# Performance work log

Measured on AMD Instinct MI355X. Metric: run time of the kernel, lower is better.

The kernel has to match this reference:

```python
import math
import jax, jax.numpy as jnp
import numpy as np

B = 32768
DM = 256      # d_model
DS = 16       # d_state
DI = 256      # d_inner (expand=1)
DTR = 16      # dt_rank = ceil(256/16)
FF = 512      # FFN hidden


def setup_inputs() -> dict:
    key = jax.random.key(0)
    ks = jax.random.split(key, 10)
    def rn(k, sh, s=0.02):
        return jax.random.normal(k, sh, jnp.float32) * s
    return {
        "x_0": jax.random.uniform(ks[0], (B, 4), jnp.float32),
        "flow_features": jax.random.normal(ks[1], (B, 1, DM), jnp.float32),
        "h": jnp.zeros((B, DI, DS), jnp.float32),
        "W_in": rn(ks[2], (2 * DI, DM)),
        "W_x": rn(ks[3], (DTR + 2 * DS, DI)),
        "W_dt": rn(ks[4], (DI, DTR)),
        "b_dt": jnp.zeros((DI,), jnp.float32),
        "A_log": jnp.log(jnp.broadcast_to(jnp.arange(1, DS + 1, dtype=jnp.float32), (DI, DS))),
        "D": jnp.ones((DI,), jnp.float32),
        "W1": rn(ks[5], (FF, DM)),
        "b1": jnp.zeros((FF,), jnp.float32),
        "W2": rn(ks[6], (DM, FF)),
        "b2": jnp.zeros((DM,), jnp.float32),
        "gamma": jnp.ones((DM,), jnp.float32),
        "beta": jnp.zeros((DM,), jnp.float32),
        "W_bb": rn(ks[7], (4, DM)),
        "b_bb": jnp.zeros((4,), jnp.float32),
    }


def _sine_embed(pos, dim_per_axis):
    # Matches gen_sineembed_for_position for pos.shape[-1]==4 (cx, cy, w, h order)
    dim_t = 10000.0 ** (2.0 * (jnp.arange(dim_per_axis) // 2).astype(jnp.float32) / dim_per_axis)
    scale = 2.0 * math.pi
    def emb(v):  # v: (b,)
        p = v[:, None] * scale / dim_t          # (b, dim)
        return jnp.stack([jnp.sin(p[:, 0::2]), jnp.cos(p[:, 1::2])], axis=2).reshape(v.shape[0], dim_per_axis)
    return jnp.concatenate([emb(pos[:, 0]), emb(pos[:, 1]), emb(pos[:, 2]), emb(pos[:, 3])], axis=1)


def reference(x_0, flow_features, h, W_in, W_x, W_dt, b_dt, A_log, D,
              W1, b1, W2, b2, gamma, beta, W_bb, b_bb):
    # 1) sinusoidal bbox embedding -> (b, d_model)
    pos = _sine_embed(x_0, DM // 4)
    # 2) in_proj + split + SiLU (l==1 so sequence dim is collapsed)
    pm = pos @ W_in.T                              # (b, 2*d_inner)
    u, gate = pm[:, :DI], pm[:, DI:]
    u = jax.nn.silu(u)
    # 3) input-dependent SSM params from flow_features (l==1)
    x_dbl = flow_features[:, 0] @ W_x.T            # (b, dt_rank + 2n)
    dlt = x_dbl[:, :DTR]
    Bm = x_dbl[:, DTR:DTR + DS]                    # (b, n)
    Cm = x_dbl[:, DTR + DS:]                       # (b, n)
    delta = jax.nn.softplus(dlt @ W_dt.T + b_dt)   # (b, d_in)
    A = -jnp.exp(A_log)                            # (d_in, n)
    # 4) single selective-scan step
    deltaA = jnp.exp(delta[:, :, None] * A)                      # (b, d_in, n)
    deltaBu = delta[:, :, None] * Bm[:, None, :] * u[:, :, None] # (b, d_in, n)
    h_new = deltaA * h + deltaBu                                 # (b, d_in, n)
    y = jnp.einsum('bdn,bn->bd', h_new, Cm) + u * D              # (b, d_in)
    # 5) gated SiLU
    y = y * jax.nn.silu(gate)                                    # (b, d_model)
    # 6) FFN + residual + LayerNorm
    src2 = jax.nn.relu(y @ W1.T + b1) @ W2.T + b2
    s = y + src2
    mu = s.mean(-1, keepdims=True)
    var = s.var(-1, keepdims=True)
    s = (s - mu) / jnp.sqrt(var + 1e-5) * gamma + beta
    # 7) bbox head + sigmoid
    out = jax.nn.sigmoid(s @ W_bb.T + b_bb)                      # (b, 4)
    return (out, h_new)
```

## Files before the change

### kernel.cpp

```cpp
#include <hip/hip_runtime.h>
#include <math.h>

#define B_TOT 32768
#define DM    256
#define DS    16
#define DI    256
#define DTR   16
#define FF    512
#define ROWS  32
#define STA   260

__device__ __forceinline__ float sigmoidf_(float x) { return 1.0f / (1.0f + __expf(-x)); }

extern "C" __global__ void __launch_bounds__(256, 3)
mamba_fused(const float* __restrict__ x0,
            const float* __restrict__ flow,
            const float* __restrict__ hin,
            const float* __restrict__ W_in,
            const float* __restrict__ W_x,
            const float* __restrict__ W_dt,
            const float* __restrict__ b_dt,
            const float* __restrict__ A_log,
            const float* __restrict__ Dp,
            const float* __restrict__ W1,
            const float* __restrict__ b1,
            const float* __restrict__ W2,
            const float* __restrict__ b2,
            const float* __restrict__ gamma,
            const float* __restrict__ beta,
            const float* __restrict__ W_bb,
            const float* __restrict__ b_bb,
            float* __restrict__ out,
            float* __restrict__ h_new)
{
    __shared__ __align__(16) float sA[ROWS * STA];
    __shared__ float sXd[ROWS * 48];
    __shared__ __align__(16) float sFF[ROWS * 64];
    __shared__ float sX0[ROWS * 4];
    __shared__ float sRed[2][ROWS * 8];
    __shared__ float sMu[ROWS], sRstd[ROWS];

    const int t = threadIdx.x;
    const size_t g0 = (size_t)blockIdx.x * ROWS;

    if (t < ROWS * 4) sX0[t] = x0[g0 * 4 + t];
    __syncthreads();

    {
        const int c = t & 63, axis = t >> 6;
        const float f = 6.28318530717958647692f * __expf(-(float)(c >> 1) * 0.2878231366242557f);
        #pragma unroll
        for (int r = 0; r < ROWS; ++r) {
            float p = sX0[r * 4 + axis] * f;
            sA[r * STA + t] = (c & 1) ? __cosf(p) : __sinf(p);
        }
    }

    for (int idx = t; idx < ROWS * 48; idx += 256) {
        const int r = idx / 48, j = idx - r * 48;
        const float4* fv = (const float4*)(flow + (g0 + r) * DM);
        const float4* wv = (const float4*)(W_x + (size_t)j * DM);
        float acc = 0.f;
        #pragma unroll 8
        for (int k = 0; k < DM / 4; ++k) {
            float4 a = fv[k], b = wv[k];
            acc += a.x * b.x + a.y * b.y + a.z * b.z + a.w * b.w;
        }
        sXd[idx] = acc;
    }
    __syncthreads();

    float u[ROWS], gate[ROWS];
    {
        float acc0[ROWS], acc1[ROWS];
        #pragma unroll
        for (int r = 0; r < ROWS; ++r) { acc0[r] = 0.f; acc1[r] = 0.f; }
        const float4* w0v = (const float4*)(W_in + (size_t)t * DM);
        const float4* w1v = (const float4*)(W_in + (size_t)(t + DI) * DM);
        #pragma unroll 2
        for (int kc = 0; kc < DM / 4; ++kc) {
            float4 w0 = w0v[kc], w1 = w1v[kc];
            #pragma unroll
            for (int r = 0; r < ROWS; ++r) {
                float4 p = *(const float4*)&sA[r * STA + kc * 4];
                acc0[r] += p.x * w0.x + p.y * w0.y + p.z * w0.z + p.w * w0.w;
                acc1[r] += p.x * w1.x + p.y * w1.y + p.z * w1.z + p.w * w1.w;
            }
        }
        #pragma unroll
        for (int r = 0; r < ROWS; ++r) {
            u[r] = acc0[r] * sigmoidf_(acc0[r]);
            gate[r] = acc1[r];
        }
    }

    float Wdt_row[DTR], Arow[DS];
    #pragma unroll
    for (int k = 0; k < DTR; ++k) Wdt_row[k] = W_dt[t * DTR + k];
    #pragma unroll
    for (int n = 0; n < DS; ++n) Arow[n] = -__expf(A_log[t * DS + n]);
    const float bdt = b_dt[t];
    const float Dt = Dp[t];

    float yv[ROWS];
    #pragma unroll
    for (int r = 0; r < ROWS; ++r) {
        const float* xd = &sXd[r * 48];
        float d = bdt;
        #pragma unroll
        for (int k = 0; k < DTR; ++k) d += xd[k] * Wdt_row[k];
        d = (d > 20.f) ? d : __logf(1.f + __expf(d));
        const float uvv = u[r];
        const size_t hbase = ((g0 + r) * DI + t) * DS;
        const float4* hv = (const float4*)(hin + hbase);
        float4* ho = (float4*)(h_new + hbase);
        float ysum = 0.f;
        #pragma unroll
        for (int n4 = 0; n4 < DS / 4; ++n4) {
            float hi[4], o[4];
            *(float4*)hi = hv[n4];
            #pragma unroll
            for (int q = 0; q < 4; ++q) {
                const int n = n4 * 4 + q;
                float dA = __expf(d * Arow[n]);
                float hn = dA * hi[q] + d * xd[16 + n] * uvv;
                o[q] = hn;
                ysum += hn * xd[32 + n];
            }
            ho[n4] = *(const float4*)o;
        }
        float yval = ysum + uvv * Dt;
        const float gt = gate[r];
        yv[r] = yval * (gt * sigmoidf_(gt));
    }

    __syncthreads();
    #pragma unroll
    for (int r = 0; r < ROWS; ++r) sA[r * STA + t] = yv[r];
    __syncthreads();

    float acc2[ROWS];
    #pragma unroll
    for (int r = 0; r < ROWS; ++r) acc2[r] = 0.f;
    const int rr = t >> 3;
    const int j8 = (t & 7) * 8;
    for (int jc = 0; jc < FF; jc += 64) {
        float fa[8];
        #pragma unroll
        for (int q = 0; q < 8; ++q) fa[q] = b1[jc + j8 + q];
        for (int kc = 0; kc < DM / 4; ++kc) {
            float4 yv4 = *(const float4*)&sA[rr * STA + kc * 4];
            #pragma unroll
            for (int q = 0; q < 8; ++q) {
                float4 w = *(const float4*)&W1[(size_t)(jc + j8 + q) * DM + kc * 4];
                fa[q] += yv4.x * w.x + yv4.y * w.y + yv4.z * w.z + yv4.w * w.w;
            }
        }
        #pragma unroll
        for (int q = 0; q < 8; ++q) sFF[rr * 64 + j8 + q] = fmaxf(fa[q], 0.f);
        __syncthreads();
        const float4* w2v = (const float4*)(W2 + (size_t)t * FF + jc);
        #pragma unroll 4
        for (int jj = 0; jj < 16; ++jj) {
            float4 w = w2v[jj];
            #pragma unroll
            for (int r = 0; r < ROWS; ++r) {
                float4 fv4 = *(const float4*)&sFF[r * 64 + jj * 4];
                acc2[r] += fv4.x * w.x + fv4.y * w.y + fv4.z * w.z + fv4.w * w.w;
            }
        }
        __syncthreads();
    }

    {
        const float b2t = b2[t];
        float sval[ROWS];
        #pragma unroll
        for (int r = 0; r < ROWS; ++r) sval[r] = sA[r * STA + t] + acc2[r] + b2t;
        __syncthreads();
        #pragma unroll
        for (int r = 0; r < ROWS; ++r) sA[r * STA + t] = sval[r];
    }
    __syncthreads();

    {
        const int r = t >> 3, q = t & 7;
        float s1 = 0.f, s2s = 0.f;
        #pragma unroll
        for (int k = 0; k < 32; ++k) {
            float v = sA[r * STA + q * 32 + k];
            s1 += v; s2s += v * v;
        }
        sRed[0][r * 8 + q] = s1;
        sRed[1][r * 8 + q] = s2s;
    }
    __syncthreads();
    if (t < ROWS) {
        float s1 = 0.f, s2s = 0.f;
        #pragma unroll
        for (int q = 0; q < 8; ++q) { s1 += sRed[0][t * 8 + q]; s2s += sRed[1][t * 8 + q]; }
        const float mu = s1 * (1.f / DM);
        const float var = s2s * (1.f / DM) - mu * mu;
        sMu[t] = mu;
        sRstd[t] = rsqrtf(var + 1e-5f);
    }
    __syncthreads();

    if (t < ROWS * 4) {
        const int r = t >> 2, c = t & 3;
        const float mu = sMu[r], rstd = sRstd[r];
        float acc = b_bb[c];
        #pragma unroll 4
        for (int i = 0; i < DM; ++i) {
            float v = (sA[r * STA + i] - mu) * rstd * gamma[i] + beta[i];
            acc += v * W_bb[c * DM + i];
        }
        out[(g0 + r) * 4 + c] = sigmoidf_(acc);
    }
}

extern "C" void kernel_launch(void* const* d_in, const int* in_sizes, int n_in,
                              void* d_out, int out_size, void* d_ws, size_t ws_size,
                              hipStream_t stream) {
    const float* x0    = (const float*)d_in[0];
    const float* flow  = (const float*)d_in[1];
    const float* hin   = (const float*)d_in[2];
    const float* W_in  = (const float*)d_in[3];
    const float* W_x   = (const float*)d_in[4];
    const float* W_dt  = (const float*)d_in[5];
    const float* b_dt  = (const float*)d_in[6];
    const float* A_log = (const float*)d_in[7];
    const float* Dp    = (const float*)d_in[8];
    const float* W1    = (const float*)d_in[9];
    const float* b1    = (const float*)d_in[10];
    const float* W2    = (const float*)d_in[11];
    const float* b2    = (const float*)d_in[12];
    const float* gamma = (const float*)d_in[13];
    const float* beta  = (const float*)d_in[14];
    const float* W_bb  = (const float*)d_in[15];
    const float* b_bb  = (const float*)d_in[16];

    float* out   = (float*)d_out;
    float* h_new = out + (size_t)B_TOT * 4;

    dim3 grid(B_TOT / ROWS), block(256);
    hipLaunchKernelGGL(mamba_fused, grid, block, 0, stream,
                       x0, flow, hin, W_in, W_x, W_dt, b_dt, A_log, Dp,
                       W1, b1, W2, b2, gamma, beta, W_bb, b_bb, out, h_new);
}
```

Before: 3.208 ms.

## Raise occupancy to four waves, shrink shared memory and FFN chunks, shuffle-based LayerNorm

Raises the launch-bounds minimum to 4 blocks per CU and cuts shared memory by reusing one buffer for the SSM parameters and the FFN hidden chunk, and by dropping the reduction buffer. The FFN chunk width goes from 64 to 32 hidden units. The gate SiLU is folded into a float2 so fewer live registers are needed. The h load is hoisted and stored as one 16-float vector, the LayerNorm reduction uses wave shuffles, and the bbox head runs on all threads with float4 loads. The tighter register budget may cause spills in the 32-row register-blocked GEMMs, and the smaller FFN chunks double the number of barriers.

```diff
diff --git a/kernel.cpp b/kernel.cpp
--- a/kernel.cpp
+++ b/kernel.cpp
@@ -12,7 +12,7 @@
 
 __device__ __forceinline__ float sigmoidf_(float x) { return 1.0f / (1.0f + __expf(-x)); }
 
-extern "C" __global__ void __launch_bounds__(256, 3)
+extern "C" __global__ void __launch_bounds__(256, 4)
 mamba_fused(const float* __restrict__ x0,
             const float* __restrict__ flow,
             const float* __restrict__ hin,
@@ -34,10 +34,8 @@
             float* __restrict__ h_new)
 {
     __shared__ __align__(16) float sA[ROWS * STA];
-    __shared__ float sXd[ROWS * 48];
-    __shared__ __align__(16) float sFF[ROWS * 64];
+    __shared__ __align__(16) float sU[ROWS * 48];
     __shared__ float sX0[ROWS * 4];
-    __shared__ float sRed[2][ROWS * 8];
     __shared__ float sMu[ROWS], sRstd[ROWS];
 
     const int t = threadIdx.x;
@@ -66,11 +64,11 @@
             float4 a = fv[k], b = wv[k];
             acc += a.x * b.x + a.y * b.y + a.z * b.z + a.w * b.w;
         }
-        sXd[idx] = acc;
-    }
-    __syncthreads();
-
-    float u[ROWS], gate[ROWS];
+        sU[idx] = acc;
+    }
+    __syncthreads();
+
+    float2 ug[ROWS];
     {
         float acc0[ROWS], acc1[ROWS];
         #pragma unroll
@@ -89,8 +87,9 @@
         }
         #pragma unroll
         for (int r = 0; r < ROWS; ++r) {
-            u[r] = acc0[r] * sigmoidf_(acc0[r]);
-            gate[r] = acc1[r];
+            float a = acc0[r], g = acc1[r];
+            ug[r].x = a * sigmoidf_(a);
+            ug[r].y = g * sigmoidf_(g);
         }
     }
 
@@ -102,70 +101,71 @@
     const float bdt = b_dt[t];
     const float Dt = Dp[t];
 
-    float yv[ROWS];
+    __syncthreads();
+
     #pragma unroll
     for (int r = 0; r < ROWS; ++r) {
-        const float* xd = &sXd[r * 48];
+        const size_t hbase = ((g0 + r) * DI + t) * DS;
+        const float4* hv = (const float4*)(hin + hbase);
+        float hi[16];
+        *(float4*)&hi[0]  = hv[0];
+        *(float4*)&hi[4]  = hv[1];
+        *(float4*)&hi[8]  = hv[2];
+        *(float4*)&hi[12] = hv[3];
+        const float* xd = &sU[r * 48];
         float d = bdt;
         #pragma unroll
         for (int k = 0; k < DTR; ++k) d += xd[k] * Wdt_row[k];
         d = (d > 20.f) ? d : __logf(1.f + __expf(d));
-        const float uvv = u[r];
-        const size_t hbase = ((g0 + r) * DI + t) * DS;
-        const float4* hv = (const float4*)(hin + hbase);
+        const float uvv = ug[r].x;
+        const float du = d * uvv;
+        float ysum = 0.f;
+        #pragma unroll
+        for (int n = 0; n < DS; ++n) {
+            float dA = __expf(d * Arow[n]);
+            float v = dA * hi[n] + du * xd[16 + n];
+            hi[n] = v;
+            ysum += v * xd[32 + n];
+        }
         float4* ho = (float4*)(h_new + hbase);
-        float ysum = 0.f;
-        #pragma unroll
-        for (int n4 = 0; n4 < DS / 4; ++n4) {
-            float hi[4], o[4];
-            *(float4*)hi = hv[n4];
-            #pragma unroll
-            for (int q = 0; q < 4; ++q) {
-                const int n = n4 * 4 + q;
-                float dA = __expf(d * Arow[n]);
-                float hn = dA * hi[q] + d * xd[16 + n] * uvv;
-                o[q] = hn;
-                ysum += hn * xd[32 + n];
-            }
-            ho[n4] = *(const float4*)o;
-        }
-        float yval = ysum + uvv * Dt;
-        const float gt = gate[r];
-        yv[r] = yval * (gt * sigmoidf_(gt));
-    }
-
-    __syncthreads();
-    #pragma unroll
-    for (int r = 0; r < ROWS; ++r) sA[r * STA + t] = yv[r];
+        ho[0] = *(const float4*)&hi[0];
+        ho[1] = *(const float4*)&hi[4];
+        ho[2] = *(const float4*)&hi[8];
+        ho[3] = *(const float4*)&hi[12];
+        sA[r * STA + t] = (ysum + uvv * Dt) * ug[r].y;
+    }
     __syncthreads();
 
     float acc2[ROWS];
     #pragma unroll
     for (int r = 0; r < ROWS; ++r) acc2[r] = 0.f;
     const int rr = t >> 3;
-    const int j8 = (t & 7) * 8;
-    for (int jc = 0; jc < FF; jc += 64) {
-        float fa[8];
-        #pragma unroll
-        for (int q = 0; q < 8; ++q) fa[q] = b1[jc + j8 + q];
+    const int j4 = (t & 7) * 4;
+    for (int jc = 0; jc < FF; jc += 32) {
+        float fa[4];
+        #pragma unroll
+        for (int q = 0; q < 4; ++q) fa[q] = b1[jc + j4 + q];
+        #pragma unroll 2
         for (int kc = 0; kc < DM / 4; ++kc) {
             float4 yv4 = *(const float4*)&sA[rr * STA + kc * 4];
             #pragma unroll
-            for (int q = 0; q < 8; ++q) {
-                float4 w = *(const float4*)&W1[(size_t)(jc + j8 + q) * DM + kc * 4];
+            for (int q = 0; q < 4; ++q) {
+                float4 w = *(const float4*)&W1[(size_t)(jc + j4 + q) * DM + kc * 4];
                 fa[q] += yv4.x * w.x + yv4.y * w.y + yv4.z * w.z + yv4.w * w.w;
             }
         }
-        #pragma unroll
-        for (int q = 0; q < 8; ++q) sFF[rr * 64 + j8 + q] = fmaxf(fa[q], 0.f);
+        float4 f4;
+        f4.x = fmaxf(fa[0], 0.f); f4.y = fmaxf(fa[1], 0.f);
+        f4.z = fmaxf(fa[2], 0.f); f4.w = fmaxf(fa[3], 0.f);
+        *(float4*)&sU[rr * 32 + j4] = f4;
         __syncthreads();
         const float4* w2v = (const float4*)(W2 + (size_t)t * FF + jc);
-        #pragma unroll 4
-        for (int jj = 0; jj < 16; ++jj) {
+        #pragma unroll
+        for (int jj = 0; jj < 8; ++jj) {
             float4 w = w2v[jj];
             #pragma unroll
             for (int r = 0; r < ROWS; ++r) {
-                float4 fv4 = *(const float4*)&sFF[r * 64 + jj * 4];
+                float4 fv4 = *(const float4*)&sU[r * 32 + jj * 4];
                 acc2[r] += fv4.x * w.x + fv4.y * w.y + fv4.z * w.z + fv4.w * w.w;
             }
         }
@@ -174,12 +174,8 @@
 
     {
         const float b2t = b2[t];
-        float sval[ROWS];
-        #pragma unroll
-        for (int r = 0; r < ROWS; ++r) sval[r] = sA[r * STA + t] + acc2[r] + b2t;
-        __syncthreads();
-        #pragma unroll
-        for (int r = 0; r < ROWS; ++r) sA[r * STA + t] = sval[r];
+        #pragma unroll
+        for (int r = 0; r < ROWS; ++r) sA[r * STA + t] += acc2[r] + b2t;
     }
     __syncthreads();
 
@@ -187,35 +183,42 @@
         const int r = t >> 3, q = t & 7;
         float s1 = 0.f, s2s = 0.f;
         #pragma unroll
-        for (int k = 0; k < 32; ++k) {
-            float v = sA[r * STA + q * 32 + k];
-            s1 += v; s2s += v * v;
-        }
-        sRed[0][r * 8 + q] = s1;
-        sRed[1][r * 8 + q] = s2s;
-    }
-    __syncthreads();
-    if (t < ROWS) {
-        float s1 = 0.f, s2s = 0.f;
-        #pragma unroll
-        for (int q = 0; q < 8; ++q) { s1 += sRed[0][t * 8 + q]; s2s += sRed[1][t * 8 + q]; }
-        const float mu = s1 * (1.f / DM);
-        const float var = s2s * (1.f / DM) - mu * mu;
-        sMu[t] = mu;
-        sRstd[t] = rsqrtf(var + 1e-5f);
-    }
-    __syncthreads();
-
-    if (t < ROWS * 4) {
-        const int r = t >> 2, c = t & 3;
+        for (int k4 = 0; k4 < 8; ++k4) {
+            float4 v = *(const float4*)&sA[r * STA + q * 32 + k4 * 4];
+            s1  += v.x + v.y + v.z + v.w;
+            s2s += v.x * v.x + v.y * v.y + v.z * v.z + v.w * v.w;
+        }
+        s1 += __shfl_xor(s1, 1);  s2s += __shfl_xor(s2s, 1);
+        s1 += __shfl_xor(s1, 2);  s2s += __shfl_xor(s2s, 2);
+        s1 += __shfl_xor(s1, 4);  s2s += __shfl_xor(s2s, 4);
+        if (q == 0) {
+            const float mu  = s1 * (1.f / DM);
+            const float var = s2s * (1.f / DM) - mu * mu;
+            sMu[r]   = mu;
+            sRstd[r] = rsqrtf(var + 1e-5f);
+        }
+    }
+    __syncthreads();
+
+    {
+        const int r = t >> 3, c = (t >> 1) & 3, hf = t & 1;
         const float mu = sMu[r], rstd = sRstd[r];
-        float acc = b_bb[c];
-        #pragma unroll 4
-        for (int i = 0; i < DM; ++i) {
-            float v = (sA[r * STA + i] - mu) * rstd * gamma[i] + beta[i];
-            acc += v * W_bb[c * DM + i];
-        }
-        out[(g0 + r) * 4 + c] = sigmoidf_(acc);
+        float acc = 0.f;
+        const int i0 = hf * 128;
+        #pragma unroll 8
+        for (int i4 = 0; i4 < 32; ++i4) {
+            const int i = i0 + i4 * 4;
+            float4 sv = *(const float4*)&sA[r * STA + i];
+            float4 gm = *(const float4*)&gamma[i];
+            float4 bt = *(const float4*)&beta[i];
+            float4 wb = *(const float4*)&W_bb[c * DM + i];
+            acc += ((sv.x - mu) * rstd * gm.x + bt.x) * wb.x
+                 + ((sv.y - mu) * rstd * gm.y + bt.y) * wb.y
+                 + ((sv.z - mu) * rstd * gm.z + bt.z) * wb.z
+                 + ((sv.w - mu) * rstd * gm.w + bt.w) * wb.w;
+        }
+        acc += __shfl_xor(acc, 1);
+        if (hf == 0) out[(g0 + r) * 4 + c] = sigmoidf_(acc + b_bb[c]);
     }
 }
 
```

Result: faster. 3.126 ms (-2.6%).
